# Kernel optimization log

Measured on AMD Instinct MI355X. Metric: run time of the kernel, lower is better.

Reference implementation:

```python
import jax, jax.numpy as jnp
import numpy as np


def _ring_indices(H, W):
    """Precompute (row, col) gather indices mapping each output element of the
    ring-unrolled image (shape H//2 x 4H) back into the HxW source image.
    Replicates the segment layout of SquareRotationalLayer exactly.
    Requires H even (odd H is out-of-bounds in the original torch code)."""
    lmid = (H - 1) // 2
    nrows = H // 2
    R = np.zeros((nrows, 4 * H), dtype=np.int32)
    Cc = np.zeros((nrows, 4 * H), dtype=np.int32)
    for dif in range(lmid + 1):
        i = lmid - dif
        el = 2 * dif if H % 2 == 1 else 2 * dif + 1
        r, c = [], []
        # seg1: top-left corner repeated i times
        r += [i] * i;                 c += [i] * i
        # seg2: top row, left->right
        r += [i] * el;                c += list(range(i, i + el))
        # seg3: top-right corner repeated 2i times
        r += [i] * (2 * i);           c += [W - i - 1] * (2 * i)
        # seg4: right column, top->bottom
        r += list(range(i, i + el));  c += [W - i - 1] * el
        # seg5: bottom-right corner repeated 2i times
        r += [i + el] * (2 * i);      c += [i + el] * (2 * i)
        # seg6: bottom row, reversed (cols i+el .. i+1)
        r += [i + el] * el;           c += list(range(i + el, i, -1))
        # seg7: bottom-left corner repeated 2i times
        r += [i + el] * (2 * i);      c += [i] * (2 * i)
        # seg8: left column, reversed (rows i+el .. i+1)
        r += list(range(i + el, i, -1)); c += [i] * el
        # seg9: top-left corner repeated i times
        r += [i] * i;                 c += [i] * i
        assert len(r) == 4 * H - 4
        R[dif, : 4 * H - 4] = r
        Cc[dif, : 4 * H - 4] = c
    # wraparound padding: last 4 columns mirror the first 4 (intent of the
    # final res[..., 4H-4:4H+4] = res[..., 0:8] line, clipped to the buffer)
    R[:, 4 * H - 4 :] = R[:, :4]
    Cc[:, 4 * H - 4 :] = Cc[:, :4]
    return R, Cc


def setup_inputs() -> dict:
    key = jax.random.key(0)
    x = jax.random.normal(key, (16, 32, 512, 512), dtype=jnp.float32)
    return {"x": x}


def reference(x) -> jnp.ndarray:
    B, C, H, W = x.shape
    R, Cc = _ring_indices(H, W)  # static shapes -> numpy at trace time is fine
    R = jnp.asarray(R)
    Cc = jnp.asarray(Cc)
    # single fused gather: (B, C, H//2, 4H)
    return x[:, :, R, Cc]
```

## Files before the change

kernel.cpp:

```cpp
#include <hip/hip_runtime.h>
#include <hip/hip_bf16.h>


#define RG_H  512
#define RG_W  512
#define RG_NR 256
#define RG_OW 2048

__device__ __forceinline__ void ring_rc(int j, int i, int el, int& r, int& c)
{
    const int cR = i + el;
    if (j >= 2044) j -= 2044;
    const int b0 = i;
    const int b1 = b0 + el;
    const int b2 = b1 + 2 * i;
    const int b3 = b2 + el;
    const int b4 = b3 + 2 * i;
    const int b5 = b4 + el;
    const int b6 = b5 + 2 * i;
    const int b7 = b6 + el;

    if (j < b0)      { r = i;              c = i;              }
    else if (j < b1) { r = i;              c = i + (j - b0);   }
    else if (j < b2) { r = i;              c = cR;             }
    else if (j < b3) { r = i + (j - b2);   c = cR;             }
    else if (j < b4) { r = cR;             c = cR;             }
    else if (j < b5) { r = cR;             c = cR - (j - b4);  }
    else if (j < b6) { r = cR;             c = i;              }
    else if (j < b7) { r = cR - (j - b6);  c = i;              }
    else             { r = i;              c = i;              }
}

__global__ __launch_bounds__(256) void SqRL_gather_kernel(
    const float* __restrict__ x, float* __restrict__ out, int total_quads)
{
    const int tid = blockIdx.x * 256 + threadIdx.x;
    if (tid >= total_quads) return;

    const int p   = tid >> 17;
    const int t   = tid & 131071;
    const int dif = t >> 9;
    const int jq  = t & 511;
    const int j0  = jq << 2;

    const int i  = 255 - dif;
    const int el = 2 * dif + 1;

    const float* __restrict__ plane = x + (size_t)p * (RG_H * RG_W);

    float4 v;
    int r, c;
    ring_rc(j0 + 0, i, el, r, c); v.x = plane[r * RG_W + c];
    ring_rc(j0 + 1, i, el, r, c); v.y = plane[r * RG_W + c];
    ring_rc(j0 + 2, i, el, r, c); v.z = plane[r * RG_W + c];
    ring_rc(j0 + 3, i, el, r, c); v.w = plane[r * RG_W + c];

    reinterpret_cast<float4*>(out)[tid] = v;
}

extern "C" void kernel_launch(void* const* d_in, const int* in_sizes, int n_in,
                              void* d_out, int out_size, void* d_ws, size_t ws_size,
                              hipStream_t stream)
{
    const float* x = (const float*)d_in[0];
    float* out = (float*)d_out;

    const int planes = in_sizes[0] / (RG_H * RG_W);
    const int total_quads = planes * RG_NR * (RG_OW / 4);
    const int blocks = (total_quads + 255) / 256;

    SqRL_gather_kernel<<<blocks, 256, 0, stream>>>(x, out, total_quads);
}
```

Measured before the change: 1.724 ms.

## Split ring gather into row kernel and LDS-transposed column kernel

The single per-element gather is split in two. A row kernel handles the top/bottom rows and corner repeats with direct row-pointer indexing and skips the quads that fall entirely inside a column segment. A second kernel fills the left and right column segments by loading 64x64 tiles coalesced into shared memory and writing them transposed. This targets the strided, uncoalesced column reads of the original gather, at the cost of a second launch, triangular masking logic, and boundary quads being written by both kernels.

```diff
diff --git a/kernel.cpp b/kernel.cpp
--- a/kernel.cpp
+++ b/kernel.cpp
@@ -1,5 +1,4 @@
 #include <hip/hip_runtime.h>
-#include <hip/hip_bf16.h>
 
 
 #define RG_H  512
@@ -7,31 +6,7 @@
 #define RG_NR 256
 #define RG_OW 2048
 
-__device__ __forceinline__ void ring_rc(int j, int i, int el, int& r, int& c)
-{
-    const int cR = i + el;
-    if (j >= 2044) j -= 2044;
-    const int b0 = i;
-    const int b1 = b0 + el;
-    const int b2 = b1 + 2 * i;
-    const int b3 = b2 + el;
-    const int b4 = b3 + 2 * i;
-    const int b5 = b4 + el;
-    const int b6 = b5 + 2 * i;
-    const int b7 = b6 + el;
-
-    if (j < b0)      { r = i;              c = i;              }
-    else if (j < b1) { r = i;              c = i + (j - b0);   }
-    else if (j < b2) { r = i;              c = cR;             }
-    else if (j < b3) { r = i + (j - b2);   c = cR;             }
-    else if (j < b4) { r = cR;             c = cR;             }
-    else if (j < b5) { r = cR;             c = cR - (j - b4);  }
-    else if (j < b6) { r = cR;             c = i;              }
-    else if (j < b7) { r = cR - (j - b6);  c = i;              }
-    else             { r = i;              c = i;              }
-}
-
-__global__ __launch_bounds__(256) void SqRL_gather_kernel(
+__global__ __launch_bounds__(256) void SqRL_rows_kernel(
     const float* __restrict__ x, float* __restrict__ out, int total_quads)
 {
     const int tid = blockIdx.x * 256 + threadIdx.x;
@@ -40,22 +15,95 @@
     const int p   = tid >> 17;
     const int t   = tid & 131071;
     const int dif = t >> 9;
-    const int jq  = t & 511;
-    const int j0  = jq << 2;
+    const int j0  = (t & 511) << 2;
+
+    const int b2 = 766 - dif, b3 = 767 + dif;
+    const int b6 = 1788 - dif, b7 = 1789 + dif;
+
+    if ((j0 >= b2 && j0 + 4 <= b3) || (j0 >= b6 && j0 + 4 <= b7)) return;
 
     const int i  = 255 - dif;
-    const int el = 2 * dif + 1;
+    const int cR = 256 + dif;
+    const int b4 = 1277 - dif;
+    const int b5 = 1278 + dif;
+
+    const float* __restrict__ rowT = x + (size_t)p * (RG_H * RG_W) + (size_t)i  * RG_W;
+    const float* __restrict__ rowB = x + (size_t)p * (RG_H * RG_W) + (size_t)cR * RG_W;
+
+    float vv[4];
+    #pragma unroll
+    for (int k = 0; k < 4; ++k) {
+        int j = j0 + k;
+        if (j >= 2044) j -= 2044;
+        float val;
+        if      (j < i)   val = rowT[i];
+        else if (j < cR)  val = rowT[j];
+        else if (j < b2)  val = rowT[cR];
+        else if (j < b3)  val = 0.0f;
+        else if (j < b4)  val = rowB[cR];
+        else if (j < b5)  val = rowB[1533 - j];
+        else if (j < b6)  val = rowB[i];
+        else if (j < b7)  val = 0.0f;
+        else              val = rowT[i];
+        vv[k] = val;
+    }
+    reinterpret_cast<float4*>(out)[tid] = make_float4(vv[0], vv[1], vv[2], vv[3]);
+}
+
+__global__ __launch_bounds__(256) void SqRL_cols_kernel(
+    const float* __restrict__ x, float* __restrict__ out)
+{
+    __shared__ float lds[64][65];
+
+    const int p    = blockIdx.y;
+    const int bx   = blockIdx.x;
+    const int side = bx >> 5;
+    const int t    = (bx >> 3) & 3;
+    const int q    = bx & 7;
+    if (q >= 2 * t + 2) return;
+
+    const int center = side ? 1788 : 766;
+    const int wr0 = t << 6;
+    const int oc0 = center - (64 * t + 63) + (q << 6);
+
+    int r0, c0;
+    if (side == 0) { r0 = oc0 - 511;  c0 = wr0 + 256; }
+    else           { r0 = 1981 - oc0; c0 = 192 - wr0; }
 
     const float* __restrict__ plane = x + (size_t)p * (RG_H * RG_W);
 
-    float4 v;
-    int r, c;
-    ring_rc(j0 + 0, i, el, r, c); v.x = plane[r * RG_W + c];
-    ring_rc(j0 + 1, i, el, r, c); v.y = plane[r * RG_W + c];
-    ring_rc(j0 + 2, i, el, r, c); v.z = plane[r * RG_W + c];
-    ring_rc(j0 + 3, i, el, r, c); v.w = plane[r * RG_W + c];
+    {
+        const int lane16 = threadIdx.x & 15;
+        const int rbase  = threadIdx.x >> 4;
+        #pragma unroll
+        for (int it = 0; it < 4; ++it) {
+            const int rr = rbase + it * 16;
+            const float4 f = *reinterpret_cast<const float4*>(
+                plane + (size_t)(r0 + rr) * RG_W + (c0 + lane16 * 4));
+            lds[rr][lane16 * 4 + 0] = f.x;
+            lds[rr][lane16 * 4 + 1] = f.y;
+            lds[rr][lane16 * 4 + 2] = f.z;
+            lds[rr][lane16 * 4 + 3] = f.w;
+        }
+    }
+    __syncthreads();
 
-    reinterpret_cast<float4*>(out)[tid] = v;
+    float* __restrict__ oplane = out + (size_t)p * (RG_NR * RG_OW);
+    const int b  = threadIdx.x & 63;
+    const int a0 = threadIdx.x >> 6;
+    const int oc = oc0 + b;
+    const int d  = oc - center;
+    const int ad = d < 0 ? -d : d;
+
+    #pragma unroll
+    for (int it = 0; it < 16; ++it) {
+        const int aa = a0 + it * 4;
+        const int wr = wr0 + aa;
+        if (ad <= wr) {
+            const float val = (side == 0) ? lds[b][aa] : lds[63 - b][63 - aa];
+            oplane[(size_t)wr * RG_OW + oc] = val;
+        }
+    }
 }
 
 extern "C" void kernel_launch(void* const* d_in, const int* in_sizes, int n_in,
@@ -67,7 +115,10 @@
 
     const int planes = in_sizes[0] / (RG_H * RG_W);
     const int total_quads = planes * RG_NR * (RG_OW / 4);
-    const int blocks = (total_quads + 255) / 256;
+    const int blocksA = (total_quads + 255) / 256;
 
-    SqRL_gather_kernel<<<blocks, 256, 0, stream>>>(x, out, total_quads);
+    SqRL_rows_kernel<<<blocksA, 256, 0, stream>>>(x, out, total_quads);
+
+    dim3 gB(64, planes);
+    SqRL_cols_kernel<<<gB, 256, 0, stream>>>(x, out);
 }
```

New measurement: 1.679 ms. 1.03x faster.
